# Optimization experiments

Hardware: AMD Instinct MI355X
Metric: run time of the kernel (lower is better)

The kernel has to match this reference:

```python
import jax, jax.numpy as jnp
import numpy as np

N_QUBITS = 10
N_LAYERS = 3
OUT_MIN, OUT_MAX = -0.1, 0.1


def _apply_1q(state, U, wire):
    # state: (B, 2**n) complex64; U: (2,2) complex64 gate on `wire` (wire 0 = MSB, PennyLane order)
    B = state.shape[0]
    s = state.reshape(B, 2 ** wire, 2, -1)
    s = jnp.einsum('ij,bljr->blir', U, s)
    return s.reshape(B, -1)


def _apply_ry_batched(state, theta, wire):
    # per-sample RY(theta) on `wire`; theta: (B,)
    B = state.shape[0]
    s = state.reshape(B, 2 ** wire, 2, -1)
    c = jnp.cos(0.5 * theta)[:, None, None]
    si = jnp.sin(0.5 * theta)[:, None, None]
    a0, a1 = s[:, :, 0, :], s[:, :, 1, :]
    s = jnp.stack([c * a0 - si * a1, si * a0 + c * a1], axis=2)
    return s.reshape(B, -1)


def _apply_cnot(state, ctrl):
    # CNOT with control=ctrl, target=ctrl+1 (adjacent wires)
    B = state.shape[0]
    s = state.reshape(B, 2 ** ctrl, 2, 2, -1)
    s = jnp.stack([s[:, :, 0], s[:, :, 1, ::-1]], axis=2)
    return s.reshape(B, -1)


def _circuit(z, weights):
    # Faithful statevector simulation of the PennyLane qnode, batched over samples.
    B = z.shape[0]
    n = N_QUBITS
    state = jnp.zeros((B, 2 ** n), jnp.complex64).at[:, 0].set(1.0)
    zc = jnp.clip(z, -1.0, 1.0)
    for i in range(n):
        state = _apply_ry_batched(state, zc[:, i % zc.shape[1]], i)
    # Fuse RZ(a)->RY(b)->RZ(c) per (layer, qubit) into one 2x2 unitary: U = Rz(c) @ Ry(b) @ Rz(a)
    a, b, c = weights[..., 0], weights[..., 1], weights[..., 2]
    ea, eap = jnp.exp(-0.5j * a), jnp.exp(0.5j * a)
    ec, ecp = jnp.exp(-0.5j * c), jnp.exp(0.5j * c)
    cb, sb = jnp.cos(0.5 * b), jnp.sin(0.5 * b)
    U = jnp.stack([jnp.stack([ec * cb * ea, -ec * sb * eap], -1),
                   jnp.stack([ecp * sb * ea, ecp * cb * eap], -1)], -2)  # (L, Q, 2, 2)
    U = U.astype(jnp.complex64)
    for l in range(N_LAYERS):
        for i in range(n):
            state = _apply_1q(state, U[l, i], i)
        for i in range(n - 1):
            state = _apply_cnot(state, i)
    probs = jnp.abs(state) ** 2  # (B, 2**n) float32
    feats = []
    for i in range(n):
        p = probs.reshape(B, 2 ** i, 2, -1)
        feats.append(p[:, :, 0].sum((1, 2)) - p[:, :, 1].sum((1, 2)))  # <Z_i>
    return jnp.stack(feats, -1)  # (B, n_qubits)


def setup_inputs() -> dict:
    key = jax.random.key(0)
    ks = jax.random.split(key, 8)
    B = 4096
    return {
        'z': jax.random.normal(ks[0], (B, N_QUBITS), jnp.float32),
        'weights': jax.random.normal(ks[1], (N_LAYERS, N_QUBITS, 3), jnp.float32) * 0.01,
        'W1': jax.random.normal(ks[2], (N_QUBITS, 32), jnp.float32) * 0.3,
        'b1': jax.random.normal(ks[3], (32,), jnp.float32) * 0.05,
        'W2': jax.random.normal(ks[4], (32, 16), jnp.float32) * 0.2,
        'b2': jax.random.normal(ks[5], (16,), jnp.float32) * 0.05,
        'W3': jax.random.normal(ks[6], (16, 1), jnp.float32) * 0.2,
        'b3': jax.random.normal(ks[7], (1,), jnp.float32) * 0.05,
    }


def reference(z, weights, W1, b1, W2, b2, W3, b3):
    feats = _circuit(z, weights)                  # (B, n_qubits)
    h = jnp.tanh(feats @ W1 + b1)
    h = jnp.tanh(h @ W2 + b2)
    raw = h @ W3 + b3                             # (B, 1)
    return jax.nn.sigmoid(raw) * (OUT_MAX - OUT_MIN) + OUT_MIN
```

## Files before the change

### kernel.cpp

```cpp
#include <hip/hip_runtime.h>

namespace {

constexpr int NQ = 10;
constexpr int NL = 3;

struct cplx { float re, im; };

__device__ __forceinline__ cplx cmul(cplx a, cplx b) {
  cplx r;
  r.re = fmaf(a.re, b.re, -a.im * b.im);
  r.im = fmaf(a.re, b.im,  a.im * b.re);
  return r;
}

__device__ __forceinline__ cplx cmadd2(cplx u, cplx a, cplx v, cplx b) {
  cplx r;
  r.re = fmaf(u.re, a.re, fmaf(-u.im, a.im, fmaf(v.re, b.re, -v.im * b.im)));
  r.im = fmaf(u.re, a.im, fmaf( u.im, a.re, fmaf(v.re, b.im,  v.im * b.re)));
  return r;
}

__device__ __forceinline__ float fast_tanh(float x) {
  float xc = fminf(fmaxf(x, -10.f), 10.f);
  float e = __expf(2.f * xc);
  return __fdividef(e - 1.f, e + 1.f);
}

__global__ __launch_bounds__(256, 4)
void qgan_kernel(const float* __restrict__ z, const float* __restrict__ wts,
                 const float* __restrict__ W1, const float* __restrict__ b1,
                 const float* __restrict__ W2, const float* __restrict__ b2,
                 const float* __restrict__ W3, const float* __restrict__ b3,
                 float* __restrict__ out, int B)
{
  const int tid  = blockIdx.x * 256 + threadIdx.x;
  const int wv   = tid >> 6;
  const int lane = threadIdx.x & 63;
  if (wv >= B) return;

  auto buildU = [&](int l, int q, cplx& u00, cplx& u01, cplx& u10, cplx& u11) {
    const float* p = wts + (l * NQ + q) * 3;
    float a = p[0], bb = p[1], cc = p[2];
    float al = 0.5f * (a + cc), be = 0.5f * (a - cc), hb = 0.5f * bb;
    float ca = __cosf(al), sa = __sinf(al);
    float cbe = __cosf(be), sbe = __sinf(be);
    float cb = __cosf(hb), sb = __sinf(hb);
    u00 = {  cb * ca, -cb * sa };
    u01 = { -sb * cbe, -sb * sbe };
    u10 = {  sb * cbe, -sb * sbe };
    u11 = {  cb * ca,  cb * sa };
  };

  cplx laneF = {1.f, 0.f};
  #pragma unroll
  for (int q = 0; q < 6; ++q) {
    float zz = z[wv * NQ + q];
    zz = fminf(fmaxf(zz, -1.f), 1.f);
    float c0 = __cosf(0.5f * zz), s0 = __sinf(0.5f * zz);
    cplx u00, u01, u10, u11; buildU(0, q, u00, u01, u10, u11);
    cplx va = { fmaf(u00.re, c0, u01.re * s0), fmaf(u00.im, c0, u01.im * s0) };
    cplx vb = { fmaf(u10.re, c0, u11.re * s0), fmaf(u10.im, c0, u11.im * s0) };
    cplx f = ((lane >> (5 - q)) & 1) ? vb : va;
    laneF = (q == 0) ? f : cmul(laneF, f);
  }
  cplx va_[4], vb_[4];
  #pragma unroll
  for (int q = 6; q < 10; ++q) {
    float zz = z[wv * NQ + q];
    zz = fminf(fmaxf(zz, -1.f), 1.f);
    float c0 = __cosf(0.5f * zz), s0 = __sinf(0.5f * zz);
    cplx u00, u01, u10, u11; buildU(0, q, u00, u01, u10, u11);
    va_[q - 6] = { fmaf(u00.re, c0, u01.re * s0), fmaf(u00.im, c0, u01.im * s0) };
    vb_[q - 6] = { fmaf(u10.re, c0, u11.re * s0), fmaf(u10.im, c0, u11.im * s0) };
  }

  cplx amp[16];
  {
    cplx P2[4];
    P2[0] = cmul(va_[2], va_[3]);
    P2[1] = cmul(va_[2], vb_[3]);
    P2[2] = cmul(vb_[2], va_[3]);
    P2[3] = cmul(vb_[2], vb_[3]);
    cplx g0 = cmul(laneF, va_[0]);
    cplx g1 = cmul(laneF, vb_[0]);
    #pragma unroll
    for (int t = 0; t < 16; ++t) {
      cplx t7 = ((t >> 2) & 1) ? vb_[1] : va_[1];
      cplx tt = cmul(t7, P2[t & 3]);
      amp[t] = cmul(((t >> 3) & 1) ? g1 : g0, tt);
    }
  }

  auto chain = [&]() {
    int src = (lane ^ (lane >> 1)) & 63;
    #pragma unroll
    for (int t = 0; t < 16; ++t) {
      amp[t].re = __shfl(amp[t].re, src);
      amp[t].im = __shfl(amp[t].im, src);
    }
    bool ctrl = (lane & 1) != 0;
    #pragma unroll
    for (int t = 0; t < 8; ++t) {
      cplx a = amp[t], b = amp[t | 8];
      amp[t]     = ctrl ? b : a;
      amp[t | 8] = ctrl ? a : b;
    }
    cplx tmp[16];
    #pragma unroll
    for (int t = 0; t < 16; ++t) tmp[t] = amp[t];
    #pragma unroll
    for (int t = 0; t < 16; ++t) amp[t] = tmp[t ^ (t >> 1)];
  };

  chain();

  #pragma unroll
  for (int l = 1; l < NL; ++l) {
    #pragma unroll
    for (int q = 0; q < NQ; ++q) {
      cplx u00, u01, u10, u11; buildU(l, q, u00, u01, u10, u11);
      const int b = 9 - q;
      if (b >= 4) {
        const int kb = b - 4;
        bool hi = ((lane >> kb) & 1) != 0;
        cplx cA = hi ? u10 : u00;
        cplx cB = hi ? u11 : u01;
        #pragma unroll
        for (int t = 0; t < 16; ++t) {
          cplx o;
          o.re = __shfl_xor(amp[t].re, 1 << kb);
          o.im = __shfl_xor(amp[t].im, 1 << kb);
          cplx a0 = hi ? o : amp[t];
          cplx a1 = hi ? amp[t] : o;
          amp[t] = cmadd2(cA, a0, cB, a1);
        }
      } else {
        const int lb = b;
        #pragma unroll
        for (int t0 = 0; t0 < 16; ++t0) {
          if (t0 & (1 << lb)) continue;
          int t1 = t0 | (1 << lb);
          cplx a0 = amp[t0], a1 = amp[t1];
          amp[t0] = cmadd2(u00, a0, u01, a1);
          amp[t1] = cmadd2(u10, a0, u11, a1);
        }
      }
    }
    if (l == 1) chain();
  }

  float p[16];
  #pragma unroll
  for (int t = 0; t < 16; ++t)
    p[t] = fmaf(amp[t].re, amp[t].re, amp[t].im * amp[t].im);

  float s_tot = 0.f, pw6 = 0.f, pw7 = 0.f, pw8 = 0.f, pw9 = 0.f;
  #pragma unroll
  for (int t = 0; t < 16; ++t) {
    s_tot += p[t];
    pw6 += (__popc(t & 0x8) & 1) ? -p[t] : p[t];
    pw7 += (__popc(t & 0xC) & 1) ? -p[t] : p[t];
    pw8 += (__popc(t & 0xE) & 1) ? -p[t] : p[t];
    pw9 += (__popc(t & 0xF) & 1) ? -p[t] : p[t];
  }

  float vals[10];
  const int   lm[10]  = {0x20, 0x30, 0x38, 0x3C, 0x3E, 0x3F, 0x3F, 0x3F, 0x3F, 0x3F};
  const float bs[10]  = {s_tot, s_tot, s_tot, s_tot, s_tot, s_tot, pw6, pw7, pw8, pw9};
  #pragma unroll
  for (int w2 = 0; w2 < 10; ++w2) {
    bool neg = (__popc(lane & lm[w2]) & 1) != 0;
    vals[w2] = neg ? -bs[w2] : bs[w2];
  }
  #pragma unroll
  for (int k = 0; k < 6; ++k) {
    #pragma unroll
    for (int w2 = 0; w2 < 10; ++w2)
      vals[w2] += __shfl_xor(vals[w2], 1 << k);
  }

  const int j = lane & 31;
  float acc = b1[j];
  #pragma unroll
  for (int i = 0; i < NQ; ++i) acc = fmaf(vals[i], W1[i * 32 + j], acc);
  float h1 = fast_tanh(acc);

  const int kk = lane & 15;
  float acc2 = b2[kk];
  #pragma unroll
  for (int jj = 0; jj < 32; ++jj) {
    float hv = __shfl(h1, jj);
    acc2 = fmaf(hv, W2[jj * 16 + kk], acc2);
  }
  float h2 = fast_tanh(acc2);

  float vv = (lane < 16) ? h2 * W3[lane] : 0.f;
  #pragma unroll
  for (int k = 0; k < 6; ++k) vv += __shfl_xor(vv, 1 << k);

  if (lane == 0) {
    float raw = vv + b3[0];
    out[wv] = 0.1f * fast_tanh(0.5f * raw);
  }
}

}

extern "C" void kernel_launch(void* const* d_in, const int* in_sizes, int n_in,
                              void* d_out, int out_size, void* d_ws, size_t ws_size,
                              hipStream_t stream) {
  const float* z   = (const float*)d_in[0];
  const float* wts = (const float*)d_in[1];
  const float* W1  = (const float*)d_in[2];
  const float* b1  = (const float*)d_in[3];
  const float* W2  = (const float*)d_in[4];
  const float* b2  = (const float*)d_in[5];
  const float* W3  = (const float*)d_in[6];
  const float* b3  = (const float*)d_in[7];
  float* out = (float*)d_out;

  int B = in_sizes[0] / NQ;
  int blocks = (B + 3) / 4;
  hipLaunchKernelGGL(qgan_kernel, dim3(blocks), dim3(256), 0, stream,
                     z, wts, W1, b1, W2, b2, W3, b3, out, B);
}
```

Measured before the change: 101.4 us.

## Absorb CNOT chains into basis relabeling and use DPP cross-lane gate exchanges

Removes the explicit CNOT-chain permutation passes by tracking the linear (XOR) basis change they induce. Later single-qubit gates become parity-masked gates applied across lane or register pairs, and the final Z expectations are read in the same transformed basis. Gate unitaries are precomputed once in a small prep kernel instead of per-wave trig. Several shuffles become DPP or readlane operations, which cuts ds_bpermute traffic. This adds a second kernel launch and intricate bit-mask bookkeeping that must be exactly right for correctness.

```diff
diff --git a/kernel.cpp b/kernel.cpp
--- a/kernel.cpp
+++ b/kernel.cpp
@@ -3,7 +3,6 @@
 namespace {
 
 constexpr int NQ = 10;
-constexpr int NL = 3;
 
 struct cplx { float re, im; };
 
@@ -21,36 +20,139 @@
   return r;
 }
 
+__device__ __forceinline__ cplx csel(bool c, cplx x, cplx y) {
+  cplx r; r.re = c ? x.re : y.re; r.im = c ? x.im : y.im; return r;
+}
+
 __device__ __forceinline__ float fast_tanh(float x) {
   float xc = fminf(fmaxf(x, -10.f), 10.f);
   float e = __expf(2.f * xc);
   return __fdividef(e - 1.f, e + 1.f);
 }
 
+template<int CTRL>
+__device__ __forceinline__ float dppf(float v) {
+  return __int_as_float(__builtin_amdgcn_update_dpp(0, __float_as_int(v), CTRL, 0xF, 0xF, true));
+}
+template<int CTRL>
+__device__ __forceinline__ cplx dppc(cplx v) { return { dppf<CTRL>(v.re), dppf<CTRL>(v.im) }; }
+
+__device__ __forceinline__ cplx shflxc(cplx v, int m) {
+  cplx r; r.re = __shfl_xor(v.re, m); r.im = __shfl_xor(v.im, m); return r;
+}
+
+__device__ __forceinline__ float rdlane(float v, int l) {
+  return __int_as_float(__builtin_amdgcn_readlane(__float_as_int(v), l));
+}
+
+__device__ __forceinline__ float wave_sum(float v) {
+  v += dppf<0xB1>(v);
+  v += dppf<0x4E>(v);
+  v += __shfl_xor(v, 4);
+  v += dppf<0x128>(v);
+  v += __shfl_xor(v, 16);
+  return rdlane(v, 0) + rdlane(v, 32);
+}
+
+__device__ __forceinline__ void loadU(const float* __restrict__ Ut, int g,
+                                      cplx& u00, cplx& u01, cplx& u10, cplx& u11) {
+  const float* p = Ut + g * 8;
+  u00 = {p[0], p[1]}; u01 = {p[2], p[3]};
+  u10 = {p[4], p[5]}; u11 = {p[6], p[7]};
+}
+
+template<int LX, int HIL>
+__device__ __forceinline__ void laneGateDS(cplx (&amp)[16], int lane,
+    cplx u00, cplx u01, cplx u10, cplx u11) {
+  bool hi = (__popc(lane & HIL) & 1) != 0;
+  cplx cA = csel(hi, u11, u00), cB = csel(hi, u10, u01);
+  #pragma unroll
+  for (int t = 0; t < 16; ++t) {
+    cplx o = shflxc(amp[t], LX);
+    amp[t] = cmadd2(cA, amp[t], cB, o);
+  }
+}
+
+template<int CTRL, int HIL>
+__device__ __forceinline__ void laneGateDPP(cplx (&amp)[16], int lane,
+    cplx u00, cplx u01, cplx u10, cplx u11) {
+  bool hi = (__popc(lane & HIL) & 1) != 0;
+  cplx cA = csel(hi, u11, u00), cB = csel(hi, u10, u01);
+  #pragma unroll
+  for (int t = 0; t < 16; ++t) {
+    cplx o = dppc<CTRL>(amp[t]);
+    amp[t] = cmadd2(cA, amp[t], cB, o);
+  }
+}
+
+template<int CTRL, int LOCX, int HIL>
+__device__ __forceinline__ void mixedGate(cplx (&amp)[16], int lane,
+    cplx u00, cplx u01, cplx u10, cplx u11) {
+  bool hi = (__popc(lane & HIL) & 1) != 0;
+  cplx cA = csel(hi, u11, u00), cB = csel(hi, u10, u01);
+  #pragma unroll
+  for (int t0 = 0; t0 < 16; ++t0) {
+    if (t0 & LOCX) continue;
+    const int t1 = t0 | LOCX;
+    cplx o0 = dppc<CTRL>(amp[t1]);
+    cplx o1 = dppc<CTRL>(amp[t0]);
+    amp[t0] = cmadd2(cA, amp[t0], cB, o0);
+    amp[t1] = cmadd2(cA, amp[t1], cB, o1);
+  }
+}
+
+constexpr int hbit(int m) { return m >= 8 ? 8 : (m >= 4 ? 4 : (m >= 2 ? 2 : 1)); }
+
+template<int PLOC, int HIL, int HILOC>
+__device__ __forceinline__ void localGate(cplx (&amp)[16], int lane,
+    cplx u00, cplx u01, cplx u10, cplx u11) {
+  bool h0 = (__popc(lane & HIL) & 1) != 0;
+  cplx cA0 = csel(h0, u11, u00), cB0 = csel(h0, u10, u01);
+  cplx cA1 = csel(h0, u00, u11), cB1 = csel(h0, u01, u10);
+  #pragma unroll
+  for (int ta = 0; ta < 16; ++ta) {
+    if (ta & hbit(PLOC)) continue;
+    const int tb = ta ^ PLOC;
+    const bool pa = (__popc(ta & HILOC) & 1) != 0;
+    cplx aA = amp[ta], aB = amp[tb];
+    if (!pa) {
+      amp[ta] = cmadd2(cA0, aA, cB0, aB);
+      amp[tb] = cmadd2(cA1, aB, cB1, aA);
+    } else {
+      amp[ta] = cmadd2(cA1, aA, cB1, aB);
+      amp[tb] = cmadd2(cA0, aB, cB0, aA);
+    }
+  }
+}
+
+__global__ void qgan_prep(const float* __restrict__ wts, float* __restrict__ U) {
+  int g = threadIdx.x;
+  if (g >= 30) return;
+  float a = wts[g * 3 + 0], b = wts[g * 3 + 1], c = wts[g * 3 + 2];
+  float al = 0.5f * (a + c), be = 0.5f * (a - c), hb = 0.5f * b;
+  float ca = cosf(al), sa = sinf(al);
+  float cbe = cosf(be), sbe = sinf(be);
+  float cb = cosf(hb), sb = sinf(hb);
+  float* p = U + g * 8;
+  p[0] =  cb * ca;  p[1] = -cb * sa;
+  p[2] = -sb * cbe; p[3] = -sb * sbe;
+  p[4] =  sb * cbe; p[5] = -sb * sbe;
+  p[6] =  cb * ca;  p[7] =  cb * sa;
+}
+
 __global__ __launch_bounds__(256, 4)
-void qgan_kernel(const float* __restrict__ z, const float* __restrict__ wts,
+void qgan_kernel(const float* __restrict__ z, const float* __restrict__ Ut,
                  const float* __restrict__ W1, const float* __restrict__ b1,
                  const float* __restrict__ W2, const float* __restrict__ b2,
                  const float* __restrict__ W3, const float* __restrict__ b3,
                  float* __restrict__ out, int B)
 {
   const int tid  = blockIdx.x * 256 + threadIdx.x;
-  const int wv   = tid >> 6;
   const int lane = threadIdx.x & 63;
+  const int wv   = __builtin_amdgcn_readfirstlane(tid >> 6);
   if (wv >= B) return;
 
-  auto buildU = [&](int l, int q, cplx& u00, cplx& u01, cplx& u10, cplx& u11) {
-    const float* p = wts + (l * NQ + q) * 3;
-    float a = p[0], bb = p[1], cc = p[2];
-    float al = 0.5f * (a + cc), be = 0.5f * (a - cc), hb = 0.5f * bb;
-    float ca = __cosf(al), sa = __sinf(al);
-    float cbe = __cosf(be), sbe = __sinf(be);
-    float cb = __cosf(hb), sb = __sinf(hb);
-    u00 = {  cb * ca, -cb * sa };
-    u01 = { -sb * cbe, -sb * sbe };
-    u10 = {  sb * cbe, -sb * sbe };
-    u11 = {  cb * ca,  cb * sa };
-  };
+  cplx u00, u01, u10, u11;
 
   cplx laneF = {1.f, 0.f};
   #pragma unroll
@@ -58,7 +160,7 @@
     float zz = z[wv * NQ + q];
     zz = fminf(fmaxf(zz, -1.f), 1.f);
     float c0 = __cosf(0.5f * zz), s0 = __sinf(0.5f * zz);
-    cplx u00, u01, u10, u11; buildU(0, q, u00, u01, u10, u11);
+    loadU(Ut, q, u00, u01, u10, u11);
     cplx va = { fmaf(u00.re, c0, u01.re * s0), fmaf(u00.im, c0, u01.im * s0) };
     cplx vb = { fmaf(u10.re, c0, u11.re * s0), fmaf(u10.im, c0, u11.im * s0) };
     cplx f = ((lane >> (5 - q)) & 1) ? vb : va;
@@ -70,7 +172,7 @@
     float zz = z[wv * NQ + q];
     zz = fminf(fmaxf(zz, -1.f), 1.f);
     float c0 = __cosf(0.5f * zz), s0 = __sinf(0.5f * zz);
-    cplx u00, u01, u10, u11; buildU(0, q, u00, u01, u10, u11);
+    loadU(Ut, q, u00, u01, u10, u11);
     va_[q - 6] = { fmaf(u00.re, c0, u01.re * s0), fmaf(u00.im, c0, u01.im * s0) };
     vb_[q - 6] = { fmaf(u10.re, c0, u11.re * s0), fmaf(u10.im, c0, u11.im * s0) };
   }
@@ -92,117 +194,73 @@
     }
   }
 
-  auto chain = [&]() {
-    int src = (lane ^ (lane >> 1)) & 63;
-    #pragma unroll
-    for (int t = 0; t < 16; ++t) {
-      amp[t].re = __shfl(amp[t].re, src);
-      amp[t].im = __shfl(amp[t].im, src);
-    }
-    bool ctrl = (lane & 1) != 0;
-    #pragma unroll
-    for (int t = 0; t < 8; ++t) {
-      cplx a = amp[t], b = amp[t | 8];
-      amp[t]     = ctrl ? b : a;
-      amp[t | 8] = ctrl ? a : b;
-    }
-    cplx tmp[16];
-    #pragma unroll
-    for (int t = 0; t < 16; ++t) tmp[t] = amp[t];
-    #pragma unroll
-    for (int t = 0; t < 16; ++t) amp[t] = tmp[t ^ (t >> 1)];
-  };
-
-  chain();
-
-  #pragma unroll
-  for (int l = 1; l < NL; ++l) {
-    #pragma unroll
-    for (int q = 0; q < NQ; ++q) {
-      cplx u00, u01, u10, u11; buildU(l, q, u00, u01, u10, u11);
-      const int b = 9 - q;
-      if (b >= 4) {
-        const int kb = b - 4;
-        bool hi = ((lane >> kb) & 1) != 0;
-        cplx cA = hi ? u10 : u00;
-        cplx cB = hi ? u11 : u01;
-        #pragma unroll
-        for (int t = 0; t < 16; ++t) {
-          cplx o;
-          o.re = __shfl_xor(amp[t].re, 1 << kb);
-          o.im = __shfl_xor(amp[t].im, 1 << kb);
-          cplx a0 = hi ? o : amp[t];
-          cplx a1 = hi ? amp[t] : o;
-          amp[t] = cmadd2(cA, a0, cB, a1);
-        }
-      } else {
-        const int lb = b;
-        #pragma unroll
-        for (int t0 = 0; t0 < 16; ++t0) {
-          if (t0 & (1 << lb)) continue;
-          int t1 = t0 | (1 << lb);
-          cplx a0 = amp[t0], a1 = amp[t1];
-          amp[t0] = cmadd2(u00, a0, u01, a1);
-          amp[t1] = cmadd2(u10, a0, u11, a1);
-        }
-      }
-    }
-    if (l == 1) chain();
-  }
+  loadU(Ut, 10, u00,u01,u10,u11); laneGateDS <0x30, 0x20>(amp, lane, u00,u01,u10,u11);
+  loadU(Ut, 11, u00,u01,u10,u11); laneGateDS <0x18, 0x30>(amp, lane, u00,u01,u10,u11);
+  loadU(Ut, 12, u00,u01,u10,u11); laneGateDS <0x0C, 0x38>(amp, lane, u00,u01,u10,u11);
+  loadU(Ut, 13, u00,u01,u10,u11); laneGateDS <0x06, 0x3C>(amp, lane, u00,u01,u10,u11);
+  loadU(Ut, 14, u00,u01,u10,u11); laneGateDPP<0x1B, 0x3E>(amp, lane, u00,u01,u10,u11);
+  loadU(Ut, 15, u00,u01,u10,u11); mixedGate  <0xB1, 8, 0x3F>(amp, lane, u00,u01,u10,u11);
+  loadU(Ut, 16, u00,u01,u10,u11); localGate  <0xC, 0x3F, 0x8>(amp, lane, u00,u01,u10,u11);
+  loadU(Ut, 17, u00,u01,u10,u11); localGate  <0x6, 0x3F, 0xC>(amp, lane, u00,u01,u10,u11);
+  loadU(Ut, 18, u00,u01,u10,u11); localGate  <0x3, 0x3F, 0xE>(amp, lane, u00,u01,u10,u11);
+  loadU(Ut, 19, u00,u01,u10,u11); localGate  <0x1, 0x3F, 0xF>(amp, lane, u00,u01,u10,u11);
+
+  loadU(Ut, 20, u00,u01,u10,u11); laneGateDS <0x28, 0x20>(amp, lane, u00,u01,u10,u11);
+  loadU(Ut, 21, u00,u01,u10,u11); laneGateDS <0x14, 0x10>(amp, lane, u00,u01,u10,u11);
+  loadU(Ut, 22, u00,u01,u10,u11); laneGateDS <0x0A, 0x28>(amp, lane, u00,u01,u10,u11);
+  loadU(Ut, 23, u00,u01,u10,u11); laneGateDS <0x05, 0x14>(amp, lane, u00,u01,u10,u11);
+  loadU(Ut, 24, u00,u01,u10,u11); mixedGate  <0x4E, 8, 0x2A>(amp, lane, u00,u01,u10,u11);
+  loadU(Ut, 25, u00,u01,u10,u11); mixedGate  <0xB1, 4, 0x15>(amp, lane, u00,u01,u10,u11);
+  loadU(Ut, 26, u00,u01,u10,u11); localGate  <0xA, 0x2A, 0x8>(amp, lane, u00,u01,u10,u11);
+  loadU(Ut, 27, u00,u01,u10,u11); localGate  <0x5, 0x15, 0x4>(amp, lane, u00,u01,u10,u11);
+  loadU(Ut, 28, u00,u01,u10,u11); localGate  <0x2, 0x2A, 0xA>(amp, lane, u00,u01,u10,u11);
+  loadU(Ut, 29, u00,u01,u10,u11); localGate  <0x1, 0x15, 0x5>(amp, lane, u00,u01,u10,u11);
 
   float p[16];
   #pragma unroll
   for (int t = 0; t < 16; ++t)
     p[t] = fmaf(amp[t].re, amp[t].re, amp[t].im * amp[t].im);
 
-  float s_tot = 0.f, pw6 = 0.f, pw7 = 0.f, pw8 = 0.f, pw9 = 0.f;
+  float s0 = 0.f, s8 = 0.f, sC = 0.f, s6 = 0.f, s3 = 0.f;
   #pragma unroll
   for (int t = 0; t < 16; ++t) {
-    s_tot += p[t];
-    pw6 += (__popc(t & 0x8) & 1) ? -p[t] : p[t];
-    pw7 += (__popc(t & 0xC) & 1) ? -p[t] : p[t];
-    pw8 += (__popc(t & 0xE) & 1) ? -p[t] : p[t];
-    pw9 += (__popc(t & 0xF) & 1) ? -p[t] : p[t];
-  }
-
-  float vals[10];
-  const int   lm[10]  = {0x20, 0x30, 0x38, 0x3C, 0x3E, 0x3F, 0x3F, 0x3F, 0x3F, 0x3F};
-  const float bs[10]  = {s_tot, s_tot, s_tot, s_tot, s_tot, s_tot, pw6, pw7, pw8, pw9};
-  #pragma unroll
-  for (int w2 = 0; w2 < 10; ++w2) {
-    bool neg = (__popc(lane & lm[w2]) & 1) != 0;
-    vals[w2] = neg ? -bs[w2] : bs[w2];
-  }
-  #pragma unroll
-  for (int k = 0; k < 6; ++k) {
-    #pragma unroll
-    for (int w2 = 0; w2 < 10; ++w2)
-      vals[w2] += __shfl_xor(vals[w2], 1 << k);
+    s0 += p[t];
+    s8 += (__popc(t & 0x8) & 1) ? -p[t] : p[t];
+    sC += (__popc(t & 0xC) & 1) ? -p[t] : p[t];
+    s6 += (__popc(t & 0x6) & 1) ? -p[t] : p[t];
+    s3 += (__popc(t & 0x3) & 1) ? -p[t] : p[t];
+  }
+
+  const int   lmask[10] = {0x20,0x30,0x18,0x0C,0x26,0x33,0x19,0x0C,0x26,0x33};
+  const float lsrc[10]  = {s0,  s0,  s0,  s0,  s0,  s0,  s8,  sC,  s6,  s3 };
+  float feats[10];
+  #pragma unroll
+  for (int w = 0; w < 10; ++w) {
+    int par = __popc(lane & lmask[w]) & 1;
+    float v = __int_as_float(__float_as_int(lsrc[w]) ^ (par << 31));
+    feats[w] = wave_sum(v);
   }
 
   const int j = lane & 31;
   float acc = b1[j];
   #pragma unroll
-  for (int i = 0; i < NQ; ++i) acc = fmaf(vals[i], W1[i * 32 + j], acc);
+  for (int i = 0; i < NQ; ++i) acc = fmaf(feats[i], W1[i * 32 + j], acc);
   float h1 = fast_tanh(acc);
 
-  const int kk = lane & 15;
-  float acc2 = b2[kk];
-  #pragma unroll
-  for (int jj = 0; jj < 32; ++jj) {
-    float hv = __shfl(h1, jj);
-    acc2 = fmaf(hv, W2[jj * 16 + kk], acc2);
-  }
+  const int k = lane & 15;
+  float acc2 = b2[k];
+  #pragma unroll
+  for (int jj = 0; jj < 32; ++jj)
+    acc2 = fmaf(rdlane(h1, jj), W2[jj * 16 + k], acc2);
   float h2 = fast_tanh(acc2);
 
-  float vv = (lane < 16) ? h2 * W3[lane] : 0.f;
-  #pragma unroll
-  for (int k = 0; k < 6; ++k) vv += __shfl_xor(vv, 1 << k);
-
-  if (lane == 0) {
-    float raw = vv + b3[0];
-    out[wv] = 0.1f * fast_tanh(0.5f * raw);
-  }
+  float vv = h2 * W3[k];
+  vv += dppf<0xB1>(vv);
+  vv += dppf<0x4E>(vv);
+  vv += __shfl_xor(vv, 4);
+  vv += dppf<0x128>(vv);
+
+  if (lane == 0) out[wv] = 0.1f * fast_tanh(0.5f * (vv + b3[0]));
 }
 
 }
@@ -219,9 +277,11 @@
   const float* W3  = (const float*)d_in[6];
   const float* b3  = (const float*)d_in[7];
   float* out = (float*)d_out;
+  float* U   = (float*)d_ws;
 
   int B = in_sizes[0] / NQ;
+  hipLaunchKernelGGL(qgan_prep, dim3(1), dim3(32), 0, stream, wts, U);
   int blocks = (B + 3) / 4;
   hipLaunchKernelGGL(qgan_kernel, dim3(blocks), dim3(256), 0, stream,
-                     z, wts, W1, b1, W2, b2, W3, b3, out, B);
-}
+                     z, U, W1, b1, W2, b2, W3, b3, out, B);
+}
```

After: 93.29 us. 8.0% less time.
